# Kernel tuning notes

Measured on AMD Instinct MI355X. Metric: run time of the kernel, lower is better.

## Reference

```python
import jax, jax.numpy as jnp
import numpy as np

B, T, D, F = 4, 1024, 256, 128  # input_dim=D, feature_dim=F, cat_size=1+F


def prelu(x, a):
    # torch.nn.PReLU with a single shared parameter (default init 0.25)
    return jnp.where(x >= 0, x, a * x)


def setup_inputs() -> dict:
    key = jax.random.key(0)
    ks = jax.random.split(key, 10)
    cat = 1 + F
    s1 = 1.0 / np.sqrt(cat)
    s2 = 1.0 / np.sqrt(F)
    return {
        "input": jax.random.normal(ks[0], (B, T, D), jnp.float32),
        "feature": jax.random.normal(ks[1], (B, T, F), jnp.float32),
        "slider": jax.random.uniform(ks[2], (B, T, 1), jnp.float32),
        "W1": jax.random.uniform(ks[3], (F, cat), jnp.float32, -s1, s1),
        "b1": jax.random.uniform(ks[4], (F,), jnp.float32, -s1, s1),
        "a1": jnp.float32(0.25),
        "W2": jax.random.uniform(ks[5], (F, F), jnp.float32, -s2, s2),
        "b2": jax.random.uniform(ks[6], (F,), jnp.float32, -s2, s2),
        "a2": jnp.float32(0.25),
        "Wp": jax.random.uniform(ks[7], (2, cat), jnp.float32, -s1, s1),
        "bp": jax.random.uniform(ks[8], (2,), jnp.float32, -s1, s1),
    }


def reference(input, feature, slider, W1, b1, a1, W2, b2, a2, Wp, bp):
    # input: (B,T,D) -> (B,T,D,1); feature broadcast over D: (B,T,1,F)
    inp = input[..., None]                       # (B,T,D,1)
    feat = feature[..., None, :]                 # (B,T,1,F)
    feat = jnp.broadcast_to(feat, (B, T, D, F))  # repeat across input_dim
    x = jnp.concatenate((inp, feat), axis=-1)    # (B,T,D,1+F)
    # tmlp: Linear -> PReLU -> Linear -> PReLU
    h = prelu(jnp.einsum('btdc,fc->btdf', x, W1) + b1, a1)  # (B,T,D,F)
    h = prelu(jnp.einsum('btdf,gf->btdg', h, W2) + b2, a2)  # (B,T,D,F)
    y = jnp.concatenate((h, inp), axis=-1)       # (B,T,D,1+F)
    p = jnp.einsum('btdc,oc->btdo', y, Wp) + bp  # (B,T,D,2)
    g = p[..., 0:1] * jax.nn.sigmoid(p[..., 1:2])  # GLU(dim=-1) -> (B,T,D,1)
    return (inp * (1.0 + g)).squeeze(-1)         # (B,T,D)
```

## Files before the change

kernel.cpp:

```cpp
#include <hip/hip_runtime.h>
#include <hip/hip_bf16.h>

#define BT 4096
#define DD 256
#define CAT 129

typedef __attribute__((ext_vector_type(8))) _Float16 f16x8;
typedef __attribute__((ext_vector_type(4))) _Float16 f16x4;
typedef __attribute__((ext_vector_type(2))) _Float16 h2;
typedef __attribute__((ext_vector_type(4))) float f32x4;

static __device__ __forceinline__ h2 cvt_pk(float a, float b) {
    return __builtin_bit_cast(h2, __builtin_amdgcn_cvt_pkrtz(a, b));
}

static __device__ __forceinline__ float fdot2f(h2 a, h2 b, float c) {
#if __has_builtin(__builtin_amdgcn_fdot2)
    return __builtin_amdgcn_fdot2(__builtin_bit_cast(__fp16 __attribute__((ext_vector_type(2))), a),
                                  __builtin_bit_cast(__fp16 __attribute__((ext_vector_type(2))), b),
                                  c, false);
#else
    return fmaf((float)a[0], (float)b[0], fmaf((float)a[1], (float)b[1], c));
#endif
}

__global__ void __launch_bounds__(256) k_cvt(
    const float* __restrict__ W1, const float* __restrict__ W2,
    _Float16* __restrict__ w2h, _Float16* __restrict__ w1h,
    _Float16* __restrict__ w10h)
{
    const int t = threadIdx.x, b = blockIdx.x;
    if (b < 8) {
        #pragma unroll
        for (int i = 0; i < 8; ++i) {
            int idx = b * 2048 + i * 256 + t;
            int g = idx >> 7;
            w2h[idx ^ ((g & 7) << 3)] = (_Float16)W2[idx];
        }
    } else {
        int q = b - 8;
        #pragma unroll
        for (int i = 0; i < 8; ++i) {
            int idx = q * 2048 + i * 256 + t;
            int f = idx >> 7, c = idx & 127;
            w1h[idx ^ ((f & 7) << 3)] = (_Float16)W1[f * CAT + 1 + c];
        }
        if (q == 0 && t < 128) w10h[t] = (_Float16)W1[t * CAT];
    }
}

__global__ void __launch_bounds__(256) k_prep2(
    const float* __restrict__ feature, const _Float16* __restrict__ w1h,
    const float* __restrict__ b1p, _Float16* __restrict__ v1h)
{
    __shared__ __align__(16) _Float16 fS[2048];
    const int t = threadIdx.x;
    const int r0 = blockIdx.x * 16;

    {
        int e = t * 8;
        int r = e >> 7, c = e & 127;
        const float4* src = (const float4*)(feature + (size_t)(r0 + r) * 128 + c);
        float4 x0 = src[0], x1 = src[1];
        f16x8 hv;
        hv[0] = (_Float16)x0.x; hv[1] = (_Float16)x0.y;
        hv[2] = (_Float16)x0.z; hv[3] = (_Float16)x0.w;
        hv[4] = (_Float16)x1.x; hv[5] = (_Float16)x1.y;
        hv[6] = (_Float16)x1.z; hv[7] = (_Float16)x1.w;
        *(f16x8*)&fS[e ^ ((r & 7) << 3)] = hv;
    }
    __syncthreads();

    const int lane = t & 63, wv = t >> 6;
    const int l15 = lane & 15, l4 = lane >> 4;

    f16x8 bfr[2][4];
    float4 b1v[2];
    #pragma unroll
    for (int nt = 0; nt < 2; ++nt) {
        const int f0 = wv * 32 + nt * 16;
        b1v[nt] = *(const float4*)(b1p + f0 + l4 * 4);
        #pragma unroll
        for (int kc = 0; kc < 4; ++kc) {
            int f = f0 + l15, c = kc * 32 + l4 * 8;
            bfr[nt][kc] = *(const f16x8*)&w1h[(f * 128 + c) ^ ((f & 7) << 3)];
        }
    }

    const f32x4 fz = {0.f, 0.f, 0.f, 0.f};
    f32x4 acc[2] = {fz, fz};
    #pragma unroll
    for (int kc = 0; kc < 4; ++kc) {
        int r = l15, c = kc * 32 + l4 * 8;
        f16x8 afr = *(const f16x8*)&fS[(r * 128 + c) ^ ((r & 7) << 3)];
        #pragma unroll
        for (int nt = 0; nt < 2; ++nt)
            acc[nt] = __builtin_amdgcn_mfma_f32_16x16x32_f16(
                bfr[nt][kc], afr, acc[nt], 0, 0, 0);
    }

    #pragma unroll
    for (int nt = 0; nt < 2; ++nt) {
        f16x4 o;
        o[0] = (_Float16)(acc[nt][0] + ((const float*)&b1v[nt])[0]);
        o[1] = (_Float16)(acc[nt][1] + ((const float*)&b1v[nt])[1]);
        o[2] = (_Float16)(acc[nt][2] + ((const float*)&b1v[nt])[2]);
        o[3] = (_Float16)(acc[nt][3] + ((const float*)&b1v[nt])[3]);
        *(f16x4*)&v1h[(size_t)(r0 + l15) * 128 + wv * 32 + nt * 16 + l4 * 4] = o;
    }
}

__global__ void __launch_bounds__(512, 4) k_main(
    const float* __restrict__ inp, const float* __restrict__ b2p,
    const float* __restrict__ Wp, const float* __restrict__ bpp,
    const float* __restrict__ a1p, const float* __restrict__ a2p,
    const _Float16* __restrict__ v1h, const _Float16* __restrict__ w2h,
    const _Float16* __restrict__ w10h, float* __restrict__ out)
{
    __shared__ __align__(16) _Float16 h1s[16384];
    __shared__ float2 prs[2][4][64];
    __shared__ float inps[512];
    __shared__ _Float16 v1s[256];
    __shared__ _Float16 w10s[128];

    const int tid  = threadIdx.x;
    const int lane = tid & 63, wv = tid >> 6;
    const int rg   = wv >> 2, cg = wv & 3;
    const int l15  = lane & 15, l4 = lane >> 4;
    const int bt0  = blockIdx.x * 2;

    #pragma unroll
    for (int q = 0; q < 4; ++q)
        ((int4*)h1s)[q * 512 + tid] = ((const int4*)w2h)[q * 512 + tid];
    inps[tid] = inp[(size_t)bt0 * DD + tid];
    if (tid < 128)
        ((unsigned*)v1s)[tid] = ((const unsigned*)(v1h + (size_t)bt0 * 128))[tid];
    else if (tid < 192)
        ((unsigned*)w10s)[tid - 128] = ((const unsigned*)w10h)[tid - 128];

    h2 z2; z2[0] = (_Float16)0.f; z2[1] = (_Float16)0.f;
    h2 a1v, a2v;
    { _Float16 x = (_Float16)a1p[0]; a1v[0] = x; a1v[1] = x; }
    { _Float16 x = (_Float16)a2p[0]; a2v[0] = x; a2v[1] = x; }
    const float wpi0 = Wp[128], wpi1 = Wp[CAT + 128];
    const float bp0  = bpp[0],  bp1  = bpp[1];

    f32x4 accInit[2];
    h2 wpa_pk[2][2], wpb_pk[2][2];
    #pragma unroll
    for (int nt = 0; nt < 2; ++nt) {
        const int g0 = cg * 32 + nt * 16 + l4 * 4;
        accInit[nt][0] = b2p[g0];     accInit[nt][1] = b2p[g0 + 1];
        accInit[nt][2] = b2p[g0 + 2]; accInit[nt][3] = b2p[g0 + 3];
        wpa_pk[nt][0] = cvt_pk(Wp[g0],           Wp[g0 + 1]);
        wpa_pk[nt][1] = cvt_pk(Wp[g0 + 2],       Wp[g0 + 3]);
        wpb_pk[nt][0] = cvt_pk(Wp[CAT + g0],     Wp[CAT + g0 + 1]);
        wpb_pk[nt][1] = cvt_pk(Wp[CAT + g0 + 2], Wp[CAT + g0 + 3]);
    }
    __syncthreads();

    f16x8 bfr[2][4];
    #pragma unroll
    for (int nt = 0; nt < 2; ++nt) {
        const int g = cg * 32 + nt * 16 + l15;
        #pragma unroll
        for (int kc = 0; kc < 4; ++kc)
            bfr[nt][kc] = *(const f16x8*)
                &h1s[(g * 128 + kc * 32 + l4 * 8) ^ ((g & 7) << 3)];
    }

    const int lr = tid >> 3, fg = tid & 7;
    h2 w10pk[8];
    #pragma unroll
    for (int m = 0; m < 8; ++m)
        w10pk[m] = *(const h2*)&w10s[fg * 16 + m * 2];

    int roff[2][4];
    #pragma unroll
    for (int rt = 0; rt < 2; ++rt) {
        const int R = rg * 32 + rt * 16 + l15;
        #pragma unroll
        for (int kc = 0; kc < 4; ++kc)
            roff[rt][kc] = (R * 128 + kc * 32 + l4 * 8) ^ ((R & 7) << 3);
    }
    const int woffA = (lr * 128 + fg * 16)     ^ ((lr & 7) << 3);
    const int woffB = (lr * 128 + fg * 16 + 8) ^ ((lr & 7) << 3);

    h2 v1pk[8];
    __syncthreads();

    #pragma unroll 2
    for (int i = 0; i < 8; ++i) {
        const int btl = i >> 2, qt = i & 3, buf = i & 1;
        if (i == 0 || i == 4) {
            #pragma unroll
            for (int m = 0; m < 8; ++m)
                v1pk[m] = *(const h2*)&v1s[btl * 128 + fg * 16 + m * 2];
        }

        {
            const float s = inps[btl * 256 + qt * 64 + lr];
            h2 s2; { _Float16 sh = (_Float16)s; s2[0] = sh; s2[1] = sh; }
            f16x8 w0, w1;
            #pragma unroll
            for (int m = 0; m < 8; ++m) {
                h2 h  = v1pk[m] + w10pk[m] * s2;
                h2 hp = __builtin_elementwise_max(h, z2)
                      + a1v * __builtin_elementwise_min(h, z2);
                if (m < 4) { w0[2 * m] = hp[0]; w0[2 * m + 1] = hp[1]; }
                else { w1[2 * (m - 4)] = hp[0]; w1[2 * (m - 4) + 1] = hp[1]; }
            }
            *(f16x8*)&h1s[buf * 8192 + woffA] = w0;
            *(f16x8*)&h1s[buf * 8192 + woffB] = w1;
        }
        __syncthreads();

        if (i > 0 && wv == (i - 1)) {
            const int pb = (i - 1) & 1, pbt = (i - 1) >> 2, pq = (i - 1) & 3;
            const float s = inps[pbt * 256 + pq * 64 + lane];
            const float2 t0 = prs[pb][0][lane], t1 = prs[pb][1][lane];
            const float2 t2 = prs[pb][2][lane], t3 = prs[pb][3][lane];
            const float e0 = t0.x + t1.x + t2.x + t3.x + wpi0 * s + bp0;
            const float e1 = t0.y + t1.y + t2.y + t3.y + wpi1 * s + bp1;
            const float gg = e0 / (1.f + __expf(-e1));
            out[(size_t)(bt0 + pbt) * DD + pq * 64 + lane] = s * (1.f + gg);
        }

        f32x4 acc[2][2];
        #pragma unroll
        for (int nt = 0; nt < 2; ++nt) {
            acc[nt][0] = accInit[nt];
            acc[nt][1] = accInit[nt];
        }
        #pragma unroll
        for (int kc = 0; kc < 4; ++kc) {
            f16x8 afr[2];
            #pragma unroll
            for (int rt = 0; rt < 2; ++rt)
                afr[rt] = *(const f16x8*)&h1s[buf * 8192 + roff[rt][kc]];
            #pragma unroll
            for (int nt = 0; nt < 2; ++nt)
                #pragma unroll
                for (int rt = 0; rt < 2; ++rt)
                    acc[nt][rt] = __builtin_amdgcn_mfma_f32_16x16x32_f16(
                        bfr[nt][kc], afr[rt], acc[nt][rt], 0, 0, 0);
        }

        #pragma unroll
        for (int rt = 0; rt < 2; ++rt) {
            float s0 = 0.f, s1 = 0.f;
            #pragma unroll
            for (int nt = 0; nt < 2; ++nt)
                #pragma unroll
                for (int p = 0; p < 2; ++p) {
                    h2 hh = cvt_pk(acc[nt][rt][2 * p], acc[nt][rt][2 * p + 1]);
                    h2 hp = __builtin_elementwise_max(hh, z2)
                          + a2v * __builtin_elementwise_min(hh, z2);
                    s0 = fdot2f(wpa_pk[nt][p], hp, s0);
                    s1 = fdot2f(wpb_pk[nt][p], hp, s1);
                }
            s0 += __shfl_xor(s0, 16); s0 += __shfl_xor(s0, 32);
            s1 += __shfl_xor(s1, 16); s1 += __shfl_xor(s1, 32);
            if (l4 == 0) {
                float2 v; v.x = s0; v.y = s1;
                prs[buf][cg][rg * 32 + rt * 16 + l15] = v;
            }
        }
    }

    __syncthreads();
    if (wv == 7) {
        const float s = inps[256 + 192 + lane];
        const float2 t0 = prs[1][0][lane], t1 = prs[1][1][lane];
        const float2 t2 = prs[1][2][lane], t3 = prs[1][3][lane];
        const float e0 = t0.x + t1.x + t2.x + t3.x + wpi0 * s + bp0;
        const float e1 = t0.y + t1.y + t2.y + t3.y + wpi1 * s + bp1;
        const float gg = e0 / (1.f + __expf(-e1));
        out[(size_t)(bt0 + 1) * DD + 192 + lane] = s * (1.f + gg);
    }
}

extern "C" void kernel_launch(void* const* d_in, const int* in_sizes, int n_in,
                              void* d_out, int out_size, void* d_ws, size_t ws_size,
                              hipStream_t stream)
{
    (void)in_sizes; (void)n_in; (void)out_size; (void)ws_size;
    const float* input   = (const float*)d_in[0];
    const float* feature = (const float*)d_in[1];
    const float* W1 = (const float*)d_in[3];
    const float* b1 = (const float*)d_in[4];
    const float* a1 = (const float*)d_in[5];
    const float* W2 = (const float*)d_in[6];
    const float* b2 = (const float*)d_in[7];
    const float* a2 = (const float*)d_in[8];
    const float* Wp = (const float*)d_in[9];
    const float* bp = (const float*)d_in[10];
    float* out = (float*)d_out;

    _Float16* v1h  = (_Float16*)d_ws;
    _Float16* w2h  = v1h + (size_t)BT * 128;
    _Float16* w1h  = w2h + 16384;
    _Float16* w10h = w1h + 16384;

    k_cvt  <<<dim3(16),   dim3(256), 0, stream>>>(W1, W2, w2h, w1h, w10h);
    k_prep2<<<dim3(256),  dim3(256), 0, stream>>>(feature, w1h, b1, v1h);
    k_main <<<dim3(2048), dim3(512), 0, stream>>>(input, b2, Wp, bp, a1, a2,
                                                  v1h, w2h, w10h, out);
}
```

Before: 63.76 us.

## Restructure main kernel to per-wave register-resident W2 with no shared memory

The main kernel is rewritten so each wave owns two (b,t) rows and keeps all of W2 in registers (32 f16x8 fragments). It computes layer-1 activations directly in registers as MFMA A-operands, which removes the LDS staging, the block-wide barriers and the cross-wave partial-sum reduction. The grid shrinks to 512 blocks of 256 threads, and Wp is pre-converted to f16 in the conversion kernel. In exchange, register pressure is much higher and occupancy is lower, and each wave runs a long serial loop of 32 iterations with small 16-row MFMA tiles. b2 and Wp are also reloaded from global memory on every iteration.

```diff
diff --git a/kernel.cpp b/kernel.cpp
--- a/kernel.cpp
+++ b/kernel.cpp
@@ -26,16 +26,17 @@
 
 __global__ void __launch_bounds__(256) k_cvt(
     const float* __restrict__ W1, const float* __restrict__ W2,
+    const float* __restrict__ Wp,
     _Float16* __restrict__ w2h, _Float16* __restrict__ w1h,
-    _Float16* __restrict__ w10h)
+    _Float16* __restrict__ w10h, _Float16* __restrict__ wpah,
+    _Float16* __restrict__ wpbh)
 {
     const int t = threadIdx.x, b = blockIdx.x;
     if (b < 8) {
         #pragma unroll
         for (int i = 0; i < 8; ++i) {
             int idx = b * 2048 + i * 256 + t;
-            int g = idx >> 7;
-            w2h[idx ^ ((g & 7) << 3)] = (_Float16)W2[idx];
+            w2h[idx] = (_Float16)W2[idx];
         }
     } else {
         int q = b - 8;
@@ -45,7 +46,11 @@
             int f = idx >> 7, c = idx & 127;
             w1h[idx ^ ((f & 7) << 3)] = (_Float16)W1[f * CAT + 1 + c];
         }
-        if (q == 0 && t < 128) w10h[t] = (_Float16)W1[t * CAT];
+        if (q == 0 && t < 128) {
+            w10h[t] = (_Float16)W1[t * CAT];
+            wpah[t] = (_Float16)Wp[t];
+            wpbh[t] = (_Float16)Wp[CAT + t];
+        }
     }
 }
 
@@ -110,173 +115,115 @@
     }
 }
 
-__global__ void __launch_bounds__(512, 4) k_main(
+__global__ void __launch_bounds__(256, 2) k_main(
     const float* __restrict__ inp, const float* __restrict__ b2p,
     const float* __restrict__ Wp, const float* __restrict__ bpp,
     const float* __restrict__ a1p, const float* __restrict__ a2p,
     const _Float16* __restrict__ v1h, const _Float16* __restrict__ w2h,
-    const _Float16* __restrict__ w10h, float* __restrict__ out)
-{
-    __shared__ __align__(16) _Float16 h1s[16384];
-    __shared__ float2 prs[2][4][64];
-    __shared__ float inps[512];
-    __shared__ _Float16 v1s[256];
-    __shared__ _Float16 w10s[128];
-
+    const _Float16* __restrict__ w10h, const _Float16* __restrict__ wpah,
+    const _Float16* __restrict__ wpbh, float* __restrict__ out)
+{
     const int tid  = threadIdx.x;
     const int lane = tid & 63, wv = tid >> 6;
-    const int rg   = wv >> 2, cg = wv & 3;
     const int l15  = lane & 15, l4 = lane >> 4;
-    const int bt0  = blockIdx.x * 2;
-
-    #pragma unroll
-    for (int q = 0; q < 4; ++q)
-        ((int4*)h1s)[q * 512 + tid] = ((const int4*)w2h)[q * 512 + tid];
-    inps[tid] = inp[(size_t)bt0 * DD + tid];
-    if (tid < 128)
-        ((unsigned*)v1s)[tid] = ((const unsigned*)(v1h + (size_t)bt0 * 128))[tid];
-    else if (tid < 192)
-        ((unsigned*)w10s)[tid - 128] = ((const unsigned*)w10h)[tid - 128];
-
+    const int w    = blockIdx.x * 4 + wv;
+    const int bt0  = w * 2;
+
+    f16x8 bfr[8][4];
+    #pragma unroll
+    for (int nt = 0; nt < 8; ++nt)
+        #pragma unroll
+        for (int kc = 0; kc < 4; ++kc)
+            bfr[nt][kc] = *(const f16x8*)
+                &w2h[(nt * 16 + l15) * 128 + kc * 32 + l4 * 8];
+
+    f16x8 w10pk[4];
+    #pragma unroll
+    for (int kc = 0; kc < 4; ++kc)
+        w10pk[kc] = *(const f16x8*)&w10h[kc * 32 + l4 * 8];
+
+    const _Float16 a1s = (_Float16)a1p[0];
+    const _Float16 a2s = (_Float16)a2p[0];
+    f16x8 a1x8 = {a1s, a1s, a1s, a1s, a1s, a1s, a1s, a1s};
+    h2 a2v; a2v[0] = a2s; a2v[1] = a2s;
+    f16x8 z8 = {(_Float16)0.f, (_Float16)0.f, (_Float16)0.f, (_Float16)0.f,
+                (_Float16)0.f, (_Float16)0.f, (_Float16)0.f, (_Float16)0.f};
     h2 z2; z2[0] = (_Float16)0.f; z2[1] = (_Float16)0.f;
-    h2 a1v, a2v;
-    { _Float16 x = (_Float16)a1p[0]; a1v[0] = x; a1v[1] = x; }
-    { _Float16 x = (_Float16)a2p[0]; a2v[0] = x; a2v[1] = x; }
     const float wpi0 = Wp[128], wpi1 = Wp[CAT + 128];
     const float bp0  = bpp[0],  bp1  = bpp[1];
-
-    f32x4 accInit[2];
-    h2 wpa_pk[2][2], wpb_pk[2][2];
-    #pragma unroll
-    for (int nt = 0; nt < 2; ++nt) {
-        const int g0 = cg * 32 + nt * 16 + l4 * 4;
-        accInit[nt][0] = b2p[g0];     accInit[nt][1] = b2p[g0 + 1];
-        accInit[nt][2] = b2p[g0 + 2]; accInit[nt][3] = b2p[g0 + 3];
-        wpa_pk[nt][0] = cvt_pk(Wp[g0],           Wp[g0 + 1]);
-        wpa_pk[nt][1] = cvt_pk(Wp[g0 + 2],       Wp[g0 + 3]);
-        wpb_pk[nt][0] = cvt_pk(Wp[CAT + g0],     Wp[CAT + g0 + 1]);
-        wpb_pk[nt][1] = cvt_pk(Wp[CAT + g0 + 2], Wp[CAT + g0 + 3]);
-    }
-    __syncthreads();
-
-    f16x8 bfr[2][4];
-    #pragma unroll
-    for (int nt = 0; nt < 2; ++nt) {
-        const int g = cg * 32 + nt * 16 + l15;
-        #pragma unroll
-        for (int kc = 0; kc < 4; ++kc)
-            bfr[nt][kc] = *(const f16x8*)
-                &h1s[(g * 128 + kc * 32 + l4 * 8) ^ ((g & 7) << 3)];
-    }
-
-    const int lr = tid >> 3, fg = tid & 7;
-    h2 w10pk[8];
-    #pragma unroll
-    for (int m = 0; m < 8; ++m)
-        w10pk[m] = *(const h2*)&w10s[fg * 16 + m * 2];
-
-    int roff[2][4];
-    #pragma unroll
-    for (int rt = 0; rt < 2; ++rt) {
-        const int R = rg * 32 + rt * 16 + l15;
-        #pragma unroll
-        for (int kc = 0; kc < 4; ++kc)
-            roff[rt][kc] = (R * 128 + kc * 32 + l4 * 8) ^ ((R & 7) << 3);
-    }
-    const int woffA = (lr * 128 + fg * 16)     ^ ((lr & 7) << 3);
-    const int woffB = (lr * 128 + fg * 16 + 8) ^ ((lr & 7) << 3);
-
-    h2 v1pk[8];
-    __syncthreads();
+    const f32x4 fz = {0.f, 0.f, 0.f, 0.f};
+
+    f16x8 v1pk[4];
+    float s_cur = inp[(size_t)bt0 * DD + l15];
 
     #pragma unroll 2
-    for (int i = 0; i < 8; ++i) {
-        const int btl = i >> 2, qt = i & 3, buf = i & 1;
-        if (i == 0 || i == 4) {
+    for (int ii = 0; ii < 32; ++ii) {
+        const int bt = bt0 + (ii >> 4), rb = ii & 15;
+
+        if ((ii & 15) == 0) {
             #pragma unroll
-            for (int m = 0; m < 8; ++m)
-                v1pk[m] = *(const h2*)&v1s[btl * 128 + fg * 16 + m * 2];
-        }
-
-        {
-            const float s = inps[btl * 256 + qt * 64 + lr];
-            h2 s2; { _Float16 sh = (_Float16)s; s2[0] = sh; s2[1] = sh; }
-            f16x8 w0, w1;
+            for (int kc = 0; kc < 4; ++kc)
+                v1pk[kc] = *(const f16x8*)
+                    &v1h[(size_t)bt * 128 + kc * 32 + l4 * 8];
+        }
+
+        const float s_row = s_cur;
+        if (ii < 31) {
+            const int jj = ii + 1;
+            s_cur = inp[(size_t)(bt0 + (jj >> 4)) * DD + (jj & 15) * 16 + l15];
+        }
+
+        const _Float16 sh = (_Float16)s_row;
+        f16x8 s8 = {sh, sh, sh, sh, sh, sh, sh, sh};
+        f16x8 afr[4];
+        #pragma unroll
+        for (int kc = 0; kc < 4; ++kc) {
+            f16x8 h = v1pk[kc] + w10pk[kc] * s8;
+            afr[kc] = __builtin_elementwise_max(h, z8)
+                    + a1x8 * __builtin_elementwise_min(h, z8);
+        }
+
+        float s0 = 0.f, s1 = 0.f;
+        #pragma unroll
+        for (int hf = 0; hf < 2; ++hf) {
+            f32x4 acc[4] = {fz, fz, fz, fz};
             #pragma unroll
-            for (int m = 0; m < 8; ++m) {
-                h2 h  = v1pk[m] + w10pk[m] * s2;
-                h2 hp = __builtin_elementwise_max(h, z2)
-                      + a1v * __builtin_elementwise_min(h, z2);
-                if (m < 4) { w0[2 * m] = hp[0]; w0[2 * m + 1] = hp[1]; }
-                else { w1[2 * (m - 4)] = hp[0]; w1[2 * (m - 4) + 1] = hp[1]; }
+            for (int kc = 0; kc < 4; ++kc)
+                #pragma unroll
+                for (int q = 0; q < 4; ++q)
+                    acc[q] = __builtin_amdgcn_mfma_f32_16x16x32_f16(
+                        bfr[hf * 4 + q][kc], afr[kc], acc[q], 0, 0, 0);
+
+            #pragma unroll
+            for (int q = 0; q < 4; ++q) {
+                const int g0 = (hf * 4 + q) * 16 + l4 * 4;
+                const float4 b2v = *(const float4*)&b2p[g0];
+                const f16x4 wa = *(const f16x4*)&wpah[g0];
+                const f16x4 wb = *(const f16x4*)&wpbh[g0];
+                h2 hh0 = cvt_pk(acc[q][0] + b2v.x, acc[q][1] + b2v.y);
+                h2 hh1 = cvt_pk(acc[q][2] + b2v.z, acc[q][3] + b2v.w);
+                h2 hp0 = __builtin_elementwise_max(hh0, z2)
+                       + a2v * __builtin_elementwise_min(hh0, z2);
+                h2 hp1 = __builtin_elementwise_max(hh1, z2)
+                       + a2v * __builtin_elementwise_min(hh1, z2);
+                h2 wa0; wa0[0] = wa[0]; wa0[1] = wa[1];
+                h2 wa1; wa1[0] = wa[2]; wa1[1] = wa[3];
+                h2 wb0; wb0[0] = wb[0]; wb0[1] = wb[1];
+                h2 wb1; wb1[0] = wb[2]; wb1[1] = wb[3];
+                s0 = fdot2f(wa0, hp0, s0); s0 = fdot2f(wa1, hp1, s0);
+                s1 = fdot2f(wb0, hp0, s1); s1 = fdot2f(wb1, hp1, s1);
             }
-            *(f16x8*)&h1s[buf * 8192 + woffA] = w0;
-            *(f16x8*)&h1s[buf * 8192 + woffB] = w1;
-        }
-        __syncthreads();
-
-        if (i > 0 && wv == (i - 1)) {
-            const int pb = (i - 1) & 1, pbt = (i - 1) >> 2, pq = (i - 1) & 3;
-            const float s = inps[pbt * 256 + pq * 64 + lane];
-            const float2 t0 = prs[pb][0][lane], t1 = prs[pb][1][lane];
-            const float2 t2 = prs[pb][2][lane], t3 = prs[pb][3][lane];
-            const float e0 = t0.x + t1.x + t2.x + t3.x + wpi0 * s + bp0;
-            const float e1 = t0.y + t1.y + t2.y + t3.y + wpi1 * s + bp1;
+        }
+
+        s0 += __shfl_xor(s0, 16); s0 += __shfl_xor(s0, 32);
+        s1 += __shfl_xor(s1, 16); s1 += __shfl_xor(s1, 32);
+
+        if (l4 == 0) {
+            const float e0 = s0 + wpi0 * s_row + bp0;
+            const float e1 = s1 + wpi1 * s_row + bp1;
             const float gg = e0 / (1.f + __expf(-e1));
-            out[(size_t)(bt0 + pbt) * DD + pq * 64 + lane] = s * (1.f + gg);
-        }
-
-        f32x4 acc[2][2];
-        #pragma unroll
-        for (int nt = 0; nt < 2; ++nt) {
-            acc[nt][0] = accInit[nt];
-            acc[nt][1] = accInit[nt];
-        }
-        #pragma unroll
-        for (int kc = 0; kc < 4; ++kc) {
-            f16x8 afr[2];
-            #pragma unroll
-            for (int rt = 0; rt < 2; ++rt)
-                afr[rt] = *(const f16x8*)&h1s[buf * 8192 + roff[rt][kc]];
-            #pragma unroll
-            for (int nt = 0; nt < 2; ++nt)
-                #pragma unroll
-                for (int rt = 0; rt < 2; ++rt)
-                    acc[nt][rt] = __builtin_amdgcn_mfma_f32_16x16x32_f16(
-                        bfr[nt][kc], afr[rt], acc[nt][rt], 0, 0, 0);
-        }
-
-        #pragma unroll
-        for (int rt = 0; rt < 2; ++rt) {
-            float s0 = 0.f, s1 = 0.f;
-            #pragma unroll
-            for (int nt = 0; nt < 2; ++nt)
-                #pragma unroll
-                for (int p = 0; p < 2; ++p) {
-                    h2 hh = cvt_pk(acc[nt][rt][2 * p], acc[nt][rt][2 * p + 1]);
-                    h2 hp = __builtin_elementwise_max(hh, z2)
-                          + a2v * __builtin_elementwise_min(hh, z2);
-                    s0 = fdot2f(wpa_pk[nt][p], hp, s0);
-                    s1 = fdot2f(wpb_pk[nt][p], hp, s1);
-                }
-            s0 += __shfl_xor(s0, 16); s0 += __shfl_xor(s0, 32);
-            s1 += __shfl_xor(s1, 16); s1 += __shfl_xor(s1, 32);
-            if (l4 == 0) {
-                float2 v; v.x = s0; v.y = s1;
-                prs[buf][cg][rg * 32 + rt * 16 + l15] = v;
-            }
-        }
-    }
-
-    __syncthreads();
-    if (wv == 7) {
-        const float s = inps[256 + 192 + lane];
-        const float2 t0 = prs[1][0][lane], t1 = prs[1][1][lane];
-        const float2 t2 = prs[1][2][lane], t3 = prs[1][3][lane];
-        const float e0 = t0.x + t1.x + t2.x + t3.x + wpi0 * s + bp0;
-        const float e1 = t0.y + t1.y + t2.y + t3.y + wpi1 * s + bp1;
-        const float gg = e0 / (1.f + __expf(-e1));
-        out[(size_t)(bt0 + 1) * DD + 192 + lane] = s * (1.f + gg);
+            out[(size_t)bt * DD + rb * 16 + l15] = s_row * (1.f + gg);
+        }
     }
 }
 
@@ -301,9 +248,12 @@
     _Float16* w2h  = v1h + (size_t)BT * 128;
     _Float16* w1h  = w2h + 16384;
     _Float16* w10h = w1h + 16384;
-
-    k_cvt  <<<dim3(16),   dim3(256), 0, stream>>>(W1, W2, w2h, w1h, w10h);
-    k_prep2<<<dim3(256),  dim3(256), 0, stream>>>(feature, w1h, b1, v1h);
-    k_main <<<dim3(2048), dim3(512), 0, stream>>>(input, b2, Wp, bp, a1, a2,
-                                                  v1h, w2h, w10h, out);
-}
+    _Float16* wpah = w10h + 128;
+    _Float16* wpbh = wpah + 128;
+
+    k_cvt  <<<dim3(16),  dim3(256), 0, stream>>>(W1, W2, Wp, w2h, w1h,
+                                                 w10h, wpah, wpbh);
+    k_prep2<<<dim3(256), dim3(256), 0, stream>>>(feature, w1h, b1, v1h);
+    k_main <<<dim3(512), dim3(256), 0, stream>>>(input, b2, Wp, bp, a1, a2,
+                                                 v1h, w2h, w10h, wpah, wpbh, out);
+}
```

New measurement: 77.35 us. +21.3%, slower.

## Build layer-1 MFMA operands in registers instead of staging through shared memory

Applied to the files above, without the earlier changes.

The main kernel no longer writes the first-layer PReLU activations into an LDS tile and reads them back. Each lane now computes its own MFMA A-fragment directly from v1, w10 and the input scalar, and loads its W2 B-fragments straight from global memory (W2 is stored unswizzled). PReLU is simplified to max(h, a*h), which matches the reference only when the slope is at most 1, as it is with the default 0.25. Most LDS traffic and the large shared buffer go away, which should raise occupancy. In exchange each lane repeats the elementwise work for its fragment, and the output write now runs right after the barrier of the same iteration instead of being deferred one step.

```diff
diff --git a/kernel.cpp b/kernel.cpp
--- a/kernel.cpp
+++ b/kernel.cpp
@@ -34,8 +34,7 @@
         #pragma unroll
         for (int i = 0; i < 8; ++i) {
             int idx = b * 2048 + i * 256 + t;
-            int g = idx >> 7;
-            w2h[idx ^ ((g & 7) << 3)] = (_Float16)W2[idx];
+            w2h[idx] = (_Float16)W2[idx];
         }
     } else {
         int q = b - 8;
@@ -117,11 +116,8 @@
     const _Float16* __restrict__ v1h, const _Float16* __restrict__ w2h,
     const _Float16* __restrict__ w10h, float* __restrict__ out)
 {
-    __shared__ __align__(16) _Float16 h1s[16384];
+    __shared__ float inps[512];
     __shared__ float2 prs[2][4][64];
-    __shared__ float inps[512];
-    __shared__ _Float16 v1s[256];
-    __shared__ _Float16 w10s[128];
 
     const int tid  = threadIdx.x;
     const int lane = tid & 63, wv = tid >> 6;
@@ -129,19 +125,25 @@
     const int l15  = lane & 15, l4 = lane >> 4;
     const int bt0  = blockIdx.x * 2;
 
-    #pragma unroll
-    for (int q = 0; q < 4; ++q)
-        ((int4*)h1s)[q * 512 + tid] = ((const int4*)w2h)[q * 512 + tid];
     inps[tid] = inp[(size_t)bt0 * DD + tid];
-    if (tid < 128)
-        ((unsigned*)v1s)[tid] = ((const unsigned*)(v1h + (size_t)bt0 * 128))[tid];
-    else if (tid < 192)
-        ((unsigned*)w10s)[tid - 128] = ((const unsigned*)w10h)[tid - 128];
-
-    h2 z2; z2[0] = (_Float16)0.f; z2[1] = (_Float16)0.f;
-    h2 a1v, a2v;
-    { _Float16 x = (_Float16)a1p[0]; a1v[0] = x; a1v[1] = x; }
-    { _Float16 x = (_Float16)a2p[0]; a2v[0] = x; a2v[1] = x; }
+
+    f16x8 bfr[2][4];
+    #pragma unroll
+    for (int nt = 0; nt < 2; ++nt)
+        #pragma unroll
+        for (int kc = 0; kc < 4; ++kc)
+            bfr[nt][kc] = *(const f16x8*)
+                &w2h[(cg * 32 + nt * 16 + l15) * 128 + kc * 32 + l4 * 8];
+
+    f16x8 w10pk[4];
+    #pragma unroll
+    for (int kc = 0; kc < 4; ++kc)
+        w10pk[kc] = *(const f16x8*)&w10h[kc * 32 + l4 * 8];
+
+    const _Float16 a1s = (_Float16)a1p[0];
+    const _Float16 a2s = (_Float16)a2p[0];
+    f16x8 a1x8 = {a1s, a1s, a1s, a1s, a1s, a1s, a1s, a1s};
+    h2 a2v; a2v[0] = a2s; a2v[1] = a2s;
     const float wpi0 = Wp[128], wpi1 = Wp[CAT + 128];
     const float bp0  = bpp[0],  bp1  = bpp[1];
 
@@ -159,124 +161,77 @@
     }
     __syncthreads();
 
-    f16x8 bfr[2][4];
-    #pragma unroll
-    for (int nt = 0; nt < 2; ++nt) {
-        const int g = cg * 32 + nt * 16 + l15;
-        #pragma unroll
-        for (int kc = 0; kc < 4; ++kc)
-            bfr[nt][kc] = *(const f16x8*)
-                &h1s[(g * 128 + kc * 32 + l4 * 8) ^ ((g & 7) << 3)];
-    }
-
-    const int lr = tid >> 3, fg = tid & 7;
-    h2 w10pk[8];
-    #pragma unroll
-    for (int m = 0; m < 8; ++m)
-        w10pk[m] = *(const h2*)&w10s[fg * 16 + m * 2];
-
-    int roff[2][4];
-    #pragma unroll
-    for (int rt = 0; rt < 2; ++rt) {
-        const int R = rg * 32 + rt * 16 + l15;
-        #pragma unroll
-        for (int kc = 0; kc < 4; ++kc)
-            roff[rt][kc] = (R * 128 + kc * 32 + l4 * 8) ^ ((R & 7) << 3);
-    }
-    const int woffA = (lr * 128 + fg * 16)     ^ ((lr & 7) << 3);
-    const int woffB = (lr * 128 + fg * 16 + 8) ^ ((lr & 7) << 3);
-
-    h2 v1pk[8];
-    __syncthreads();
+    f16x8 v1pk[4];
 
     #pragma unroll 2
     for (int i = 0; i < 8; ++i) {
         const int btl = i >> 2, qt = i & 3, buf = i & 1;
-        if (i == 0 || i == 4) {
+
+        if ((i & 3) == 0) {
             #pragma unroll
-            for (int m = 0; m < 8; ++m)
-                v1pk[m] = *(const h2*)&v1s[btl * 128 + fg * 16 + m * 2];
-        }
-
-        {
-            const float s = inps[btl * 256 + qt * 64 + lr];
-            h2 s2; { _Float16 sh = (_Float16)s; s2[0] = sh; s2[1] = sh; }
-            f16x8 w0, w1;
+            for (int kc = 0; kc < 4; ++kc)
+                v1pk[kc] = *(const f16x8*)
+                    &v1h[(size_t)(bt0 + btl) * 128 + kc * 32 + l4 * 8];
+        }
+
+        const int rbase = btl * 256 + qt * 64 + rg * 32;
+        const float s0f = inps[rbase + l15];
+        const float s1f = inps[rbase + 16 + l15];
+        const _Float16 sh0 = (_Float16)s0f, sh1 = (_Float16)s1f;
+        f16x8 s8a = {sh0, sh0, sh0, sh0, sh0, sh0, sh0, sh0};
+        f16x8 s8b = {sh1, sh1, sh1, sh1, sh1, sh1, sh1, sh1};
+
+        f32x4 acc[2][2];
+        acc[0][0] = accInit[0]; acc[0][1] = accInit[0];
+        acc[1][0] = accInit[1]; acc[1][1] = accInit[1];
+
+        #pragma unroll
+        for (int kc = 0; kc < 4; ++kc) {
+            f16x8 h0 = v1pk[kc] + w10pk[kc] * s8a;
+            f16x8 af0 = __builtin_elementwise_max(h0, a1x8 * h0);
+            f16x8 h1 = v1pk[kc] + w10pk[kc] * s8b;
+            f16x8 af1 = __builtin_elementwise_max(h1, a1x8 * h1);
             #pragma unroll
-            for (int m = 0; m < 8; ++m) {
-                h2 h  = v1pk[m] + w10pk[m] * s2;
-                h2 hp = __builtin_elementwise_max(h, z2)
-                      + a1v * __builtin_elementwise_min(h, z2);
-                if (m < 4) { w0[2 * m] = hp[0]; w0[2 * m + 1] = hp[1]; }
-                else { w1[2 * (m - 4)] = hp[0]; w1[2 * (m - 4) + 1] = hp[1]; }
+            for (int nt = 0; nt < 2; ++nt) {
+                acc[nt][0] = __builtin_amdgcn_mfma_f32_16x16x32_f16(
+                    bfr[nt][kc], af0, acc[nt][0], 0, 0, 0);
+                acc[nt][1] = __builtin_amdgcn_mfma_f32_16x16x32_f16(
+                    bfr[nt][kc], af1, acc[nt][1], 0, 0, 0);
             }
-            *(f16x8*)&h1s[buf * 8192 + woffA] = w0;
-            *(f16x8*)&h1s[buf * 8192 + woffB] = w1;
+        }
+
+        #pragma unroll
+        for (int rt = 0; rt < 2; ++rt) {
+            float p0 = 0.f, p1 = 0.f;
+            #pragma unroll
+            for (int nt = 0; nt < 2; ++nt) {
+                h2 hh0 = cvt_pk(acc[nt][rt][0], acc[nt][rt][1]);
+                h2 hh1 = cvt_pk(acc[nt][rt][2], acc[nt][rt][3]);
+                h2 hp0 = __builtin_elementwise_max(hh0, a2v * hh0);
+                h2 hp1 = __builtin_elementwise_max(hh1, a2v * hh1);
+                p0 = fdot2f(wpa_pk[nt][0], hp0, p0);
+                p0 = fdot2f(wpa_pk[nt][1], hp1, p0);
+                p1 = fdot2f(wpb_pk[nt][0], hp0, p1);
+                p1 = fdot2f(wpb_pk[nt][1], hp1, p1);
+            }
+            p0 += __shfl_xor(p0, 16); p0 += __shfl_xor(p0, 32);
+            p1 += __shfl_xor(p1, 16); p1 += __shfl_xor(p1, 32);
+            if (l4 == 0) {
+                float2 v; v.x = p0; v.y = p1;
+                prs[buf][cg][rg * 32 + rt * 16 + l15] = v;
+            }
         }
         __syncthreads();
 
-        if (i > 0 && wv == (i - 1)) {
-            const int pb = (i - 1) & 1, pbt = (i - 1) >> 2, pq = (i - 1) & 3;
-            const float s = inps[pbt * 256 + pq * 64 + lane];
-            const float2 t0 = prs[pb][0][lane], t1 = prs[pb][1][lane];
-            const float2 t2 = prs[pb][2][lane], t3 = prs[pb][3][lane];
+        if (wv == i) {
+            const float s = inps[btl * 256 + qt * 64 + lane];
+            const float2 t0 = prs[buf][0][lane], t1 = prs[buf][1][lane];
+            const float2 t2 = prs[buf][2][lane], t3 = prs[buf][3][lane];
             const float e0 = t0.x + t1.x + t2.x + t3.x + wpi0 * s + bp0;
             const float e1 = t0.y + t1.y + t2.y + t3.y + wpi1 * s + bp1;
             const float gg = e0 / (1.f + __expf(-e1));
-            out[(size_t)(bt0 + pbt) * DD + pq * 64 + lane] = s * (1.f + gg);
-        }
-
-        f32x4 acc[2][2];
-        #pragma unroll
-        for (int nt = 0; nt < 2; ++nt) {
-            acc[nt][0] = accInit[nt];
-            acc[nt][1] = accInit[nt];
-        }
-        #pragma unroll
-        for (int kc = 0; kc < 4; ++kc) {
-            f16x8 afr[2];
-            #pragma unroll
-            for (int rt = 0; rt < 2; ++rt)
-                afr[rt] = *(const f16x8*)&h1s[buf * 8192 + roff[rt][kc]];
-            #pragma unroll
-            for (int nt = 0; nt < 2; ++nt)
-                #pragma unroll
-                for (int rt = 0; rt < 2; ++rt)
-                    acc[nt][rt] = __builtin_amdgcn_mfma_f32_16x16x32_f16(
-                        bfr[nt][kc], afr[rt], acc[nt][rt], 0, 0, 0);
-        }
-
-        #pragma unroll
-        for (int rt = 0; rt < 2; ++rt) {
-            float s0 = 0.f, s1 = 0.f;
-            #pragma unroll
-            for (int nt = 0; nt < 2; ++nt)
-                #pragma unroll
-                for (int p = 0; p < 2; ++p) {
-                    h2 hh = cvt_pk(acc[nt][rt][2 * p], acc[nt][rt][2 * p + 1]);
-                    h2 hp = __builtin_elementwise_max(hh, z2)
-                          + a2v * __builtin_elementwise_min(hh, z2);
-                    s0 = fdot2f(wpa_pk[nt][p], hp, s0);
-                    s1 = fdot2f(wpb_pk[nt][p], hp, s1);
-                }
-            s0 += __shfl_xor(s0, 16); s0 += __shfl_xor(s0, 32);
-            s1 += __shfl_xor(s1, 16); s1 += __shfl_xor(s1, 32);
-            if (l4 == 0) {
-                float2 v; v.x = s0; v.y = s1;
-                prs[buf][cg][rg * 32 + rt * 16 + l15] = v;
-            }
-        }
-    }
-
-    __syncthreads();
-    if (wv == 7) {
-        const float s = inps[256 + 192 + lane];
-        const float2 t0 = prs[1][0][lane], t1 = prs[1][1][lane];
-        const float2 t2 = prs[1][2][lane], t3 = prs[1][3][lane];
-        const float e0 = t0.x + t1.x + t2.x + t3.x + wpi0 * s + bp0;
-        const float e1 = t0.y + t1.y + t2.y + t3.y + wpi1 * s + bp1;
-        const float gg = e0 / (1.f + __expf(-e1));
-        out[(size_t)(bt0 + 1) * DD + 192 + lane] = s * (1.f + gg);
+            out[(size_t)(bt0 + btl) * DD + qt * 64 + lane] = s * (1.f + gg);
+        }
     }
 }
 
```

After: 71.60 us. 12.3% more time.
